# Performance work log

Measured on AMD Instinct MI355X. Metric: run time of the kernel, lower is better.

## Reference

```python
import jax, jax.numpy as jnp
import numpy as np

N_NODES = 100000
N_EDGES = 3200000
BATCH = 256
NUM_TAU = 4
ORDER = 8


def setup_inputs() -> dict:
    key = jax.random.key(0)
    k1, k2, k3, k4, k5 = jax.random.split(key, 5)
    coeffs = jax.random.normal(k1, (NUM_TAU, ORDER + 1), dtype=jnp.float32)
    # positive weights mimicking a degree-normalized adjacency
    edge_weights = jax.random.uniform(k2, (N_EDGES,), dtype=jnp.float32)
    src = jax.random.randint(k3, (N_EDGES,), 0, N_NODES, dtype=jnp.int32)
    dst = jax.random.randint(k4, (N_EDGES,), 0, N_NODES, dtype=jnp.int32)
    batch_indices = jax.random.randint(k5, (BATCH,), 0, N_NODES, dtype=jnp.int64)
    return {
        "coeffs": coeffs,
        "edge_weights": edge_weights,
        "src": src,
        "dst": dst,
        "batch_indices": batch_indices,
        "n_nodes": N_NODES,
    }


def reference(coeffs, edge_weights, src, dst, batch_indices, n_nodes):
    # coeffs: [num_tau, order+1]; edge list defines sparse normalized adjacency.
    B = batch_indices.shape[0]
    order = coeffs.shape[1] - 1
    # _create_batch: one-hot columns, monome[batch_indices[j], j] = 1
    monome = jnp.zeros((n_nodes, B), dtype=coeffs.dtype)
    monome = monome.at[batch_indices, jnp.arange(B)].set(1.0)
    # out[t] = sum_k coeffs[t, k] * A^k @ one_hot
    out = coeffs[:, 0][:, None, None] * monome[None, :, :]
    for k in range(order):
        # SpMM: monome_new[d] += w_e * monome[s] for each edge e=(s,d)
        monome = jax.ops.segment_sum(
            edge_weights[:, None] * monome[src], dst, num_segments=n_nodes
        )
        out = out + coeffs[:, k + 1][:, None, None] * monome[None, :, :]
    return out
```

## Files before the change

### kernel.cpp

```cpp
#include <hip/hip_runtime.h>

#define N_NODES 100000
#define BATCH   256
#define NUM_TAU 4
#define ORDER   8
#define NB      ((size_t)N_NODES * BATCH)
#define NBUK    98
#define NBLK    391

__device__ __forceinline__ unsigned short f2bf(float f) {
    unsigned int u = __float_as_uint(f);
    u += 0x7FFFu + ((u >> 16) & 1u);
    return (unsigned short)(u >> 16);
}
__device__ __forceinline__ float bf2f(unsigned short h) {
    return __uint_as_float((unsigned int)h << 16);
}


__global__ void hist_kernel(const int* __restrict__ dst, int* __restrict__ counts, int E) {
    int e = blockIdx.x * blockDim.x + threadIdx.x;
    if (e < E) atomicAdd(&counts[dst[e]], 1);
}

__global__ void scan1(const int* __restrict__ counts, int* __restrict__ blockSum) {
    __shared__ int s[256];
    int n = blockIdx.x * 256 + threadIdx.x;
    s[threadIdx.x] = (n < N_NODES) ? counts[n] : 0;
    __syncthreads();
    for (int st = 128; st > 0; st >>= 1) {
        if (threadIdx.x < st) s[threadIdx.x] += s[threadIdx.x + st];
        __syncthreads();
    }
    if (threadIdx.x == 0) blockSum[blockIdx.x] = s[0];
}

__global__ void scan2(int* __restrict__ blockSum) {
    __shared__ int s[512];
    int t = threadIdx.x;
    int v = (t < NBLK) ? blockSum[t] : 0;
    s[t] = v;
    __syncthreads();
    for (int st = 1; st < 512; st <<= 1) {
        int u = (t >= st) ? s[t - st] : 0;
        __syncthreads();
        s[t] += u;
        __syncthreads();
    }
    if (t < NBLK) blockSum[t] = s[t] - v;
}

__global__ void scan3(const int* __restrict__ counts, const int* __restrict__ blockSumEx,
                      int* __restrict__ rowStart) {
    __shared__ int s[256];
    int n = blockIdx.x * 256 + threadIdx.x;
    int v = (n < N_NODES) ? counts[n] : 0;
    s[threadIdx.x] = v;
    __syncthreads();
    for (int st = 1; st < 256; st <<= 1) {
        int u = (threadIdx.x >= st) ? s[threadIdx.x - st] : 0;
        __syncthreads();
        s[threadIdx.x] += u;
        __syncthreads();
    }
    if (n < N_NODES) rowStart[n] = blockSumEx[blockIdx.x] + s[threadIdx.x] - v;
}

__global__ void initcur_kernel(const int* __restrict__ rowStart, int* __restrict__ cursor,
                               int* __restrict__ bcur) {
    int n = blockIdx.x * 256 + threadIdx.x;
    if (n < N_NODES) cursor[n] = rowStart[n];
    if (n < NBUK) bcur[n] = rowStart[n << 10];
}

#define EPT 16
__global__ void bucketize_kernel(const int* __restrict__ src, const int* __restrict__ dst,
                                 const float* __restrict__ w, int* __restrict__ bcur,
                                 int2* __restrict__ isw, int* __restrict__ idn, int E) {
    __shared__ int cnt[NBUK], base[NBUK], off[NBUK];
    int e0 = blockIdx.x * (256 * EPT);
    for (int i = threadIdx.x; i < NBUK; i += 256) { cnt[i] = 0; off[i] = 0; }
    __syncthreads();
    #pragma unroll
    for (int i = 0; i < EPT; ++i) {
        int e = e0 + i * 256 + threadIdx.x;
        if (e < E) atomicAdd(&cnt[dst[e] >> 10], 1);
    }
    __syncthreads();
    for (int i = threadIdx.x; i < NBUK; i += 256) {
        int c = cnt[i];
        base[i] = c ? atomicAdd(&bcur[i], c) : 0;
    }
    __syncthreads();
    #pragma unroll
    for (int i = 0; i < EPT; ++i) {
        int e = e0 + i * 256 + threadIdx.x;
        if (e < E) {
            int d = dst[e];
            int b = d >> 10;
            int p = base[b] + atomicAdd(&off[b], 1);
            isw[p] = make_int2(src[e], __float_as_int(w[e]));
            idn[p] = d;
        }
    }
}

__global__ void place_kernel(const int2* __restrict__ isw, const int* __restrict__ idn,
                             int* __restrict__ cursor, int2* __restrict__ csr_pair, int E) {
    int e = blockIdx.x * blockDim.x + threadIdx.x;
    if (e < E) {
        int d = idn[e];
        int p = atomicAdd(&cursor[d], 1);
        csr_pair[p] = isw[e];
    }
}


__global__ void colmap_kernel(const int* __restrict__ bi, int* __restrict__ col_of_node,
                              int* __restrict__ next_dup) {
    int j = threadIdx.x;
    int prev = atomicExch(&col_of_node[bi[j]], j);
    next_dup[j] = prev;
}

__global__ void m1_edges_kernel(const int* __restrict__ src, const int* __restrict__ dst,
                                const float* __restrict__ w,
                                const int* __restrict__ col_of_node,
                                const int* __restrict__ next_dup,
                                float* __restrict__ m1, int* __restrict__ flag, int E) {
    int e = blockIdx.x * blockDim.x + threadIdx.x;
    if (e >= E) return;
    int j = col_of_node[src[e]];
    if (j < 0) return;
    float we = w[e];
    int d = dst[e];
    flag[d] = 1;
    size_t rb = (size_t)d * BATCH;
    while (j >= 0) {
        atomicAdd(&m1[rb + j], we);
        j = next_dup[j];
    }
}

__global__ void spmm_k2(const float* __restrict__ m1, unsigned short* __restrict__ m2,
                        const int* __restrict__ rowStart, const int* __restrict__ counts,
                        const int2* __restrict__ csr_pair, const int* __restrict__ flag) {
    int wave = threadIdx.x >> 6;
    int lane = threadIdx.x & 63;
    int node = blockIdx.x * 4 + wave;
    if (node >= N_NODES) return;
    int col0 = lane * 4;

    int start = rowStart[node];
    int len   = counts[node];

    float4 acc = make_float4(0.f, 0.f, 0.f, 0.f);
    for (int i = 0; i < len; ++i) {
        int2 pr = csr_pair[start + i];
        if (flag[pr.x]) {
            float w = __int_as_float(pr.y);
            float4 v = *(const float4*)(m1 + (size_t)pr.x * BATCH + col0);
            acc.x += w * v.x; acc.y += w * v.y; acc.z += w * v.z; acc.w += w * v.w;
        }
    }
    ushort4 o;
    o.x = f2bf(acc.x); o.y = f2bf(acc.y); o.z = f2bf(acc.z); o.w = f2bf(acc.w);
    *(ushort4*)(m2 + (size_t)node * BATCH + col0) = o;
}

__global__ void spmm_bf(const unsigned short* __restrict__ min_, unsigned short* __restrict__ mout,
                        const int* __restrict__ rowStart, const int* __restrict__ counts,
                        const int2* __restrict__ csr_pair) {
    int wave = threadIdx.x >> 6;
    int lane = threadIdx.x & 63;
    int node = blockIdx.x * 4 + wave;
    if (node >= N_NODES) return;
    int col0 = lane * 4;

    int start = rowStart[node];
    int len   = counts[node];

    float4 acc = make_float4(0.f, 0.f, 0.f, 0.f);
    int i = 0;
    for (; i + 8 <= len; i += 8) {
        int2 pr[8];
        #pragma unroll
        for (int u = 0; u < 8; ++u) pr[u] = csr_pair[start + i + u];
        ushort4 v[8];
        #pragma unroll
        for (int u = 0; u < 8; ++u)
            v[u] = *(const ushort4*)(min_ + (size_t)pr[u].x * BATCH + col0);
        #pragma unroll
        for (int u = 0; u < 8; ++u) {
            float w = __int_as_float(pr[u].y);
            acc.x += w * bf2f(v[u].x);
            acc.y += w * bf2f(v[u].y);
            acc.z += w * bf2f(v[u].z);
            acc.w += w * bf2f(v[u].w);
        }
    }
    for (; i < len; ++i) {
        int2 pr = csr_pair[start + i];
        float w = __int_as_float(pr.y);
        ushort4 v = *(const ushort4*)(min_ + (size_t)pr.x * BATCH + col0);
        acc.x += w * bf2f(v.x);
        acc.y += w * bf2f(v.y);
        acc.z += w * bf2f(v.z);
        acc.w += w * bf2f(v.w);
    }
    ushort4 o;
    o.x = f2bf(acc.x); o.y = f2bf(acc.y); o.z = f2bf(acc.z); o.w = f2bf(acc.w);
    *(ushort4*)(mout + (size_t)node * BATCH + col0) = o;
}

__global__ void combine_bf(float* __restrict__ out, const unsigned short* __restrict__ m28,
                           const float* __restrict__ coeffs, const int* __restrict__ bi) {
    size_t tid = (size_t)blockIdx.x * blockDim.x + threadIdx.x;
    size_t base = tid * 4;
    if (base >= NB) return;
    int node = (int)(base >> 8);
    int j0   = (int)(base & 255);

    float4 p[ORDER];
    p[0] = *(const float4*)(out + base);
    #pragma unroll
    for (int k = 2; k <= ORDER; ++k) {
        ushort4 v = *(const ushort4*)(m28 + (size_t)(k - 2) * NB + base);
        p[k - 1] = make_float4(bf2f(v.x), bf2f(v.y), bf2f(v.z), bf2f(v.w));
    }

    float oh[4];
    #pragma unroll
    for (int i = 0; i < 4; ++i) oh[i] = (bi[j0 + i] == node) ? 1.0f : 0.0f;

    #pragma unroll
    for (int t = 0; t < NUM_TAU; ++t) {
        float c0 = coeffs[t * (ORDER + 1)];
        float4 o = make_float4(c0 * oh[0], c0 * oh[1], c0 * oh[2], c0 * oh[3]);
        #pragma unroll
        for (int k = 1; k <= ORDER; ++k) {
            float c = coeffs[t * (ORDER + 1) + k];
            o.x += c * p[k - 1].x;
            o.y += c * p[k - 1].y;
            o.z += c * p[k - 1].z;
            o.w += c * p[k - 1].w;
        }
        *(float4*)(out + (size_t)t * NB + base) = o;
    }
}


__global__ void spmm_half(const float* __restrict__ min_, float* __restrict__ mout,
                          const int* __restrict__ rowStart, const int* __restrict__ counts,
                          const int2* __restrict__ csr_pair, int colOff) {
    int wave = threadIdx.x >> 6;
    int lane = threadIdx.x & 63;
    int node = blockIdx.x * 4 + wave;
    if (node >= N_NODES) return;
    int c = colOff + lane * 2;
    int start = rowStart[node];
    int len   = counts[node];
    float2 acc = make_float2(0.f, 0.f);
    int i = 0;
    for (; i + 8 <= len; i += 8) {
        int2 pr[8];
        #pragma unroll
        for (int u = 0; u < 8; ++u) pr[u] = csr_pair[start + i + u];
        float2 v[8];
        #pragma unroll
        for (int u = 0; u < 8; ++u)
            v[u] = *(const float2*)(min_ + (size_t)pr[u].x * BATCH + c);
        #pragma unroll
        for (int u = 0; u < 8; ++u) {
            float w = __int_as_float(pr[u].y);
            acc.x += w * v[u].x;
            acc.y += w * v[u].y;
        }
    }
    for (; i < len; ++i) {
        int2 pr = csr_pair[start + i];
        float w = __int_as_float(pr.y);
        float2 v = *(const float2*)(min_ + (size_t)pr.x * BATCH + c);
        acc.x += w * v.x;
        acc.y += w * v.y;
    }
    *(float2*)(mout + (size_t)node * BATCH + c) = acc;
}

__global__ void combine_kernel(float* __restrict__ out, const float* __restrict__ m14,
                               const float* __restrict__ coeffs, const int* __restrict__ bi) {
    size_t tid = (size_t)blockIdx.x * blockDim.x + threadIdx.x;
    size_t base = tid * 4;
    if (base >= NB) return;
    int node = (int)(base >> 8);
    int j0   = (int)(base & 255);
    float4 p[ORDER];
    #pragma unroll
    for (int k = 1; k <= 4; ++k)
        p[k - 1] = *(const float4*)(m14 + (size_t)(k - 1) * NB + base);
    #pragma unroll
    for (int k = 5; k <= 8; ++k)
        p[k - 1] = *(const float4*)(out + (size_t)(k - 5) * NB + base);
    float oh[4];
    #pragma unroll
    for (int i = 0; i < 4; ++i) oh[i] = (bi[j0 + i] == node) ? 1.0f : 0.0f;
    #pragma unroll
    for (int t = 0; t < NUM_TAU; ++t) {
        float c0 = coeffs[t * (ORDER + 1)];
        float4 o = make_float4(c0 * oh[0], c0 * oh[1], c0 * oh[2], c0 * oh[3]);
        #pragma unroll
        for (int k = 1; k <= ORDER; ++k) {
            float c = coeffs[t * (ORDER + 1) + k];
            o.x += c * p[k - 1].x;
            o.y += c * p[k - 1].y;
            o.z += c * p[k - 1].z;
            o.w += c * p[k - 1].w;
        }
        *(float4*)(out + (size_t)t * NB + base) = o;
    }
}

extern "C" void kernel_launch(void* const* d_in, const int* in_sizes, int n_in,
                              void* d_out, int out_size, void* d_ws, size_t ws_size,
                              hipStream_t stream) {
    const float* coeffs = (const float*)d_in[0];
    const float* ew     = (const float*)d_in[1];
    const int*   src    = (const int*)d_in[2];
    const int*   dst    = (const int*)d_in[3];
    const int*   bi     = (const int*)d_in[4];
    const int E = in_sizes[1];

    float* out = (float*)d_out;

    auto align_up = [](uintptr_t v, uintptr_t a) { return (v + a - 1) & ~(a - 1); };

    uintptr_t p0 = (uintptr_t)d_ws;
    int* counts      = (int*)p0;  p0 += (size_t)N_NODES * 4;  p0 = align_up(p0, 256);
    int* rowStart    = (int*)p0;  p0 += (size_t)N_NODES * 4;  p0 = align_up(p0, 256);
    int* cursor      = (int*)p0;  p0 += (size_t)N_NODES * 4;  p0 = align_up(p0, 256);
    int* blockSum    = (int*)p0;  p0 += (size_t)NBLK * 4;     p0 = align_up(p0, 256);
    int* bcur        = (int*)p0;  p0 += (size_t)NBUK * 4;     p0 = align_up(p0, 256);
    int* col_of_node = (int*)p0;  p0 += (size_t)N_NODES * 4;  p0 = align_up(p0, 256);
    int* next_dup    = (int*)p0;  p0 += 1024;                 p0 = align_up(p0, 256);
    int* flag        = (int*)p0;  p0 += (size_t)N_NODES * 4;  p0 = align_up(p0, 256);
    int2* csr_pair   = (int2*)p0; p0 += (size_t)E * 8;        p0 = align_up(p0, 256);
    void* big        = (void*)p0;
    size_t big_bytes = ((uintptr_t)d_ws + ws_size > p0) ? ((uintptr_t)d_ws + ws_size - p0) : 0;

    int eb = (E + 255) / 256;
    int nodeGrid = (N_NODES + 3) / 4;
    int cgrid = (int)((NB / 4 + 255) / 256);

    bool schemeA = (big_bytes >= 7 * NB * 2);
    uintptr_t ibase;
    if (schemeA) ibase = (uintptr_t)big + 5 * NB * 2;
    else         ibase = (uintptr_t)big + 3 * NB * 4;
    ibase = align_up(ibase, 256);
    int2* isw = (int2*)ibase;
    int*  idn = (int*)(ibase + (size_t)E * 8);

    hipMemsetAsync(counts, 0, (size_t)N_NODES * 4, stream);
    hist_kernel<<<eb, 256, 0, stream>>>(dst, counts, E);
    scan1<<<NBLK, 256, 0, stream>>>(counts, blockSum);
    scan2<<<1, 512, 0, stream>>>(blockSum);
    scan3<<<NBLK, 256, 0, stream>>>(counts, blockSum, rowStart);
    initcur_kernel<<<NBLK, 256, 0, stream>>>(rowStart, cursor, bcur);
    bucketize_kernel<<<(E + 256 * EPT - 1) / (256 * EPT), 256, 0, stream>>>(
        src, dst, ew, bcur, isw, idn, E);
    place_kernel<<<eb, 256, 0, stream>>>(isw, idn, cursor, csr_pair, E);

    if (schemeA) {
        unsigned short* m28 = (unsigned short*)big;
        float* m1 = out;

        hipMemsetAsync(col_of_node, 0xFF, (size_t)N_NODES * 4, stream);
        hipMemsetAsync(flag, 0, (size_t)N_NODES * 4, stream);
        hipMemsetAsync(m1, 0, NB * 4, stream);

        colmap_kernel<<<1, 256, 0, stream>>>(bi, col_of_node, next_dup);
        m1_edges_kernel<<<eb, 256, 0, stream>>>(src, dst, ew, col_of_node, next_dup,
                                                m1, flag, E);
        spmm_k2<<<nodeGrid, 256, 0, stream>>>(m1, m28, rowStart, counts, csr_pair, flag);
        for (int k = 3; k <= ORDER; ++k) {
            spmm_bf<<<nodeGrid, 256, 0, stream>>>(m28 + (size_t)(k - 3) * NB,
                                                  m28 + (size_t)(k - 2) * NB,
                                                  rowStart, counts, csr_pair);
        }
        combine_bf<<<cgrid, 256, 0, stream>>>(out, m28, coeffs, bi);
    } else {
        float* fbig = (float*)big;
        float* mpow[ORDER + 1];
        for (int k = 1; k <= 4; ++k) mpow[k] = fbig + (size_t)(k - 1) * NB;
        for (int k = 5; k <= 8; ++k) mpow[k] = out + (size_t)(k - 5) * NB;

        hipMemsetAsync(col_of_node, 0xFF, (size_t)N_NODES * 4, stream);
        hipMemsetAsync(flag, 0, (size_t)N_NODES * 4, stream);
        hipMemsetAsync(mpow[1], 0, NB * 4, stream);
        colmap_kernel<<<1, 256, 0, stream>>>(bi, col_of_node, next_dup);
        m1_edges_kernel<<<eb, 256, 0, stream>>>(src, dst, ew, col_of_node, next_dup,
                                                mpow[1], flag, E);
        for (int h = 0; h < 2; ++h) {
            int colOff = h * 128;
            for (int k = 2; k <= ORDER; ++k) {
                spmm_half<<<nodeGrid, 256, 0, stream>>>(mpow[k - 1], mpow[k],
                                                        rowStart, counts, csr_pair, colOff);
            }
        }
        combine_kernel<<<cgrid, 256, 0, stream>>>(out, fbig, coeffs, bi);
    }
}
```

Before: 2.022 ms.

## Bucket edges by (dst block, src block) segments so CSR rows are src-sorted

Replaces the per-block dst-bucket scatter with a two-level (dst>>10, src>>10) segment histogram, a per-dst-bucket scan, and a global-atomic scatter into those segments. Edges in each CSR row then come out roughly ordered by source block, which should give the SpMM gathers better cache locality. The cost is a second atomic in the histogram, global atomics on about 9.6k counters in place of shared-memory local offsets, and an extra scan kernel.

```diff
diff --git a/kernel.cpp b/kernel.cpp
--- a/kernel.cpp
+++ b/kernel.cpp
@@ -6,6 +6,7 @@
 #define ORDER   8
 #define NB      ((size_t)N_NODES * BATCH)
 #define NBUK    98
+#define NSEG    (NBUK * NBUK)
 #define NBLK    391
 
 __device__ __forceinline__ unsigned short f2bf(float f) {
@@ -18,9 +19,14 @@
 }
 
 
-__global__ void hist_kernel(const int* __restrict__ dst, int* __restrict__ counts, int E) {
+__global__ void hist_kernel(const int* __restrict__ src, const int* __restrict__ dst,
+                            int* __restrict__ counts, int* __restrict__ segCnt, int E) {
     int e = blockIdx.x * blockDim.x + threadIdx.x;
-    if (e < E) atomicAdd(&counts[dst[e]], 1);
+    if (e < E) {
+        int d = dst[e];
+        atomicAdd(&counts[d], 1);
+        atomicAdd(&segCnt[(d >> 10) * NBUK + (src[e] >> 10)], 1);
+    }
 }
 
 __global__ void scan1(const int* __restrict__ counts, int* __restrict__ blockSum) {
@@ -66,42 +72,37 @@
     if (n < N_NODES) rowStart[n] = blockSumEx[blockIdx.x] + s[threadIdx.x] - v;
 }
 
-__global__ void initcur_kernel(const int* __restrict__ rowStart, int* __restrict__ cursor,
-                               int* __restrict__ bcur) {
+__global__ void initcur_kernel(const int* __restrict__ rowStart, int* __restrict__ cursor) {
     int n = blockIdx.x * 256 + threadIdx.x;
     if (n < N_NODES) cursor[n] = rowStart[n];
-    if (n < NBUK) bcur[n] = rowStart[n << 10];
-}
-
-#define EPT 16
-__global__ void bucketize_kernel(const int* __restrict__ src, const int* __restrict__ dst,
-                                 const float* __restrict__ w, int* __restrict__ bcur,
-                                 int2* __restrict__ isw, int* __restrict__ idn, int E) {
-    __shared__ int cnt[NBUK], base[NBUK], off[NBUK];
-    int e0 = blockIdx.x * (256 * EPT);
-    for (int i = threadIdx.x; i < NBUK; i += 256) { cnt[i] = 0; off[i] = 0; }
+}
+
+__global__ void segscan_kernel(const int* __restrict__ segCnt, const int* __restrict__ rowStart,
+                               int* __restrict__ segCur) {
+    __shared__ int s[128];
+    int b = blockIdx.x;
+    int t = threadIdx.x;
+    int v = (t < NBUK) ? segCnt[b * NBUK + t] : 0;
+    s[t] = v;
     __syncthreads();
-    #pragma unroll
-    for (int i = 0; i < EPT; ++i) {
-        int e = e0 + i * 256 + threadIdx.x;
-        if (e < E) atomicAdd(&cnt[dst[e] >> 10], 1);
-    }
-    __syncthreads();
-    for (int i = threadIdx.x; i < NBUK; i += 256) {
-        int c = cnt[i];
-        base[i] = c ? atomicAdd(&bcur[i], c) : 0;
-    }
-    __syncthreads();
-    #pragma unroll
-    for (int i = 0; i < EPT; ++i) {
-        int e = e0 + i * 256 + threadIdx.x;
-        if (e < E) {
-            int d = dst[e];
-            int b = d >> 10;
-            int p = base[b] + atomicAdd(&off[b], 1);
-            isw[p] = make_int2(src[e], __float_as_int(w[e]));
-            idn[p] = d;
-        }
+    for (int st = 1; st < 128; st <<= 1) {
+        int u = (t >= st) ? s[t - st] : 0;
+        __syncthreads();
+        s[t] += u;
+        __syncthreads();
+    }
+    if (t < NBUK) segCur[b * NBUK + t] = rowStart[b << 10] + s[t] - v;
+}
+
+__global__ void scatter2_kernel(const int* __restrict__ src, const int* __restrict__ dst,
+                                const float* __restrict__ w, int* __restrict__ segCur,
+                                int2* __restrict__ isw, int* __restrict__ idn, int E) {
+    int e = blockIdx.x * blockDim.x + threadIdx.x;
+    if (e < E) {
+        int s0 = src[e], d = dst[e];
+        int p = atomicAdd(&segCur[(d >> 10) * NBUK + (s0 >> 10)], 1);
+        isw[p] = make_int2(s0, __float_as_int(w[e]));
+        idn[p] = d;
     }
 }
 
@@ -339,7 +340,8 @@
     int* rowStart    = (int*)p0;  p0 += (size_t)N_NODES * 4;  p0 = align_up(p0, 256);
     int* cursor      = (int*)p0;  p0 += (size_t)N_NODES * 4;  p0 = align_up(p0, 256);
     int* blockSum    = (int*)p0;  p0 += (size_t)NBLK * 4;     p0 = align_up(p0, 256);
-    int* bcur        = (int*)p0;  p0 += (size_t)NBUK * 4;     p0 = align_up(p0, 256);
+    int* segCnt      = (int*)p0;  p0 += (size_t)NSEG * 4;     p0 = align_up(p0, 256);
+    int* segCur      = (int*)p0;  p0 += (size_t)NSEG * 4;     p0 = align_up(p0, 256);
     int* col_of_node = (int*)p0;  p0 += (size_t)N_NODES * 4;  p0 = align_up(p0, 256);
     int* next_dup    = (int*)p0;  p0 += 1024;                 p0 = align_up(p0, 256);
     int* flag        = (int*)p0;  p0 += (size_t)N_NODES * 4;  p0 = align_up(p0, 256);
@@ -360,13 +362,14 @@
     int*  idn = (int*)(ibase + (size_t)E * 8);
 
     hipMemsetAsync(counts, 0, (size_t)N_NODES * 4, stream);
-    hist_kernel<<<eb, 256, 0, stream>>>(dst, counts, E);
+    hipMemsetAsync(segCnt, 0, (size_t)NSEG * 4, stream);
+    hist_kernel<<<eb, 256, 0, stream>>>(src, dst, counts, segCnt, E);
     scan1<<<NBLK, 256, 0, stream>>>(counts, blockSum);
     scan2<<<1, 512, 0, stream>>>(blockSum);
     scan3<<<NBLK, 256, 0, stream>>>(counts, blockSum, rowStart);
-    initcur_kernel<<<NBLK, 256, 0, stream>>>(rowStart, cursor, bcur);
-    bucketize_kernel<<<(E + 256 * EPT - 1) / (256 * EPT), 256, 0, stream>>>(
-        src, dst, ew, bcur, isw, idn, E);
+    initcur_kernel<<<NBLK, 256, 0, stream>>>(rowStart, cursor);
+    segscan_kernel<<<NBUK, 128, 0, stream>>>(segCnt, rowStart, segCur);
+    scatter2_kernel<<<eb, 256, 0, stream>>>(src, dst, ew, segCur, isw, idn, E);
     place_kernel<<<eb, 256, 0, stream>>>(isw, idn, cursor, csr_pair, E);
 
     if (schemeA) {
```

Result: slower. 2.340 ms (+15.7%).

## Slice bf16 monome buffers into 16-column panels for cache-resident SpMM gathers

Applied to the files above, without the earlier changes.

Stores the bf16 power matrices as 16 column slices of 16 columns each, so each slice (about 3.2 MB) can stay resident in cache while the SpMM kernel gathers neighbor rows. The new SpMM launches slice-major blocks in which each wave handles 12 rows, with lanes split into 8 edge groups by 8 column pairs, followed by a shuffle reduction. The aim is to turn random 512-byte row gathers from a 51 MB matrix into cache-hitting 32-byte gathers. The trade-off is that CSR indices and weights are now re-read once per slice, 16 times in total, and combine and spmm_k2 must use the sliced addressing.

```diff
diff --git a/kernel.cpp b/kernel.cpp
--- a/kernel.cpp
+++ b/kernel.cpp
@@ -7,6 +7,11 @@
 #define NB      ((size_t)N_NODES * BATCH)
 #define NBUK    98
 #define NBLK    391
+#define SLICES  16
+#define SCOLS   16
+#define NB_SL   ((size_t)N_NODES * SCOLS)
+#define RPW     12
+#define CHUNKS  2084
 
 __device__ __forceinline__ unsigned short f2bf(float f) {
     unsigned int u = __float_as_uint(f);
@@ -165,52 +170,65 @@
     }
     ushort4 o;
     o.x = f2bf(acc.x); o.y = f2bf(acc.y); o.z = f2bf(acc.z); o.w = f2bf(acc.w);
-    *(ushort4*)(m2 + (size_t)node * BATCH + col0) = o;
-}
-
-__global__ void spmm_bf(const unsigned short* __restrict__ min_, unsigned short* __restrict__ mout,
-                        const int* __restrict__ rowStart, const int* __restrict__ counts,
-                        const int2* __restrict__ csr_pair) {
+    int slice = col0 >> 4;
+    int off   = col0 & 15;
+    *(ushort4*)(m2 + (size_t)slice * NB_SL + (size_t)node * SCOLS + off) = o;
+}
+
+__global__ void spmm_bf_slice(const unsigned short* __restrict__ min_,
+                              unsigned short* __restrict__ mout,
+                              const int* __restrict__ rowStart, const int* __restrict__ counts,
+                              const int2* __restrict__ csr_pair) {
+    int slice = blockIdx.x / CHUNKS;
+    int chunk = blockIdx.x - slice * CHUNKS;
     int wave = threadIdx.x >> 6;
     int lane = threadIdx.x & 63;
-    int node = blockIdx.x * 4 + wave;
-    if (node >= N_NODES) return;
-    int col0 = lane * 4;
-
-    int start = rowStart[node];
-    int len   = counts[node];
-
-    float4 acc = make_float4(0.f, 0.f, 0.f, 0.f);
-    int i = 0;
-    for (; i + 8 <= len; i += 8) {
-        int2 pr[8];
-        #pragma unroll
-        for (int u = 0; u < 8; ++u) pr[u] = csr_pair[start + i + u];
-        ushort4 v[8];
-        #pragma unroll
-        for (int u = 0; u < 8; ++u)
-            v[u] = *(const ushort4*)(min_ + (size_t)pr[u].x * BATCH + col0);
-        #pragma unroll
-        for (int u = 0; u < 8; ++u) {
-            float w = __int_as_float(pr[u].y);
-            acc.x += w * bf2f(v[u].x);
-            acc.y += w * bf2f(v[u].y);
-            acc.z += w * bf2f(v[u].z);
-            acc.w += w * bf2f(v[u].w);
-        }
-    }
-    for (; i < len; ++i) {
-        int2 pr = csr_pair[start + i];
-        float w = __int_as_float(pr.y);
-        ushort4 v = *(const ushort4*)(min_ + (size_t)pr.x * BATCH + col0);
-        acc.x += w * bf2f(v.x);
-        acc.y += w * bf2f(v.y);
-        acc.z += w * bf2f(v.z);
-        acc.w += w * bf2f(v.w);
-    }
-    ushort4 o;
-    o.x = f2bf(acc.x); o.y = f2bf(acc.y); o.z = f2bf(acc.z); o.w = f2bf(acc.w);
-    *(ushort4*)(mout + (size_t)node * BATCH + col0) = o;
+    int g = lane >> 3;
+    int c = lane & 7;
+
+    const unsigned short* msl = min_ + (size_t)slice * NB_SL;
+    unsigned short*       osl = mout + (size_t)slice * NB_SL;
+
+    int node0 = (chunk * 4 + wave) * RPW;
+    for (int r = 0; r < RPW; ++r) {
+        int node = node0 + r;
+        if (node >= N_NODES) return;
+        int start = rowStart[node];
+        int len   = counts[node];
+        float ax = 0.f, ay = 0.f;
+        int i = 0;
+        for (; i + 32 <= len; i += 32) {
+            int2 pr0 = csr_pair[start + i + g];
+            int2 pr1 = csr_pair[start + i + 8 + g];
+            int2 pr2 = csr_pair[start + i + 16 + g];
+            int2 pr3 = csr_pair[start + i + 24 + g];
+            unsigned int v0 = *(const unsigned int*)(msl + (size_t)pr0.x * SCOLS + c * 2);
+            unsigned int v1 = *(const unsigned int*)(msl + (size_t)pr1.x * SCOLS + c * 2);
+            unsigned int v2 = *(const unsigned int*)(msl + (size_t)pr2.x * SCOLS + c * 2);
+            unsigned int v3 = *(const unsigned int*)(msl + (size_t)pr3.x * SCOLS + c * 2);
+            float w0 = __int_as_float(pr0.y), w1 = __int_as_float(pr1.y);
+            float w2 = __int_as_float(pr2.y), w3 = __int_as_float(pr3.y);
+            ax += w0 * bf2f((unsigned short)v0); ay += w0 * bf2f((unsigned short)(v0 >> 16));
+            ax += w1 * bf2f((unsigned short)v1); ay += w1 * bf2f((unsigned short)(v1 >> 16));
+            ax += w2 * bf2f((unsigned short)v2); ay += w2 * bf2f((unsigned short)(v2 >> 16));
+            ax += w3 * bf2f((unsigned short)v3); ay += w3 * bf2f((unsigned short)(v3 >> 16));
+        }
+        for (; i < len; i += 8) {
+            int e = i + g;
+            int s0 = 0; float w = 0.f;
+            if (e < len) { int2 pr = csr_pair[start + e]; s0 = pr.x; w = __int_as_float(pr.y); }
+            unsigned int v = *(const unsigned int*)(msl + (size_t)s0 * SCOLS + c * 2);
+            ax += w * bf2f((unsigned short)v);
+            ay += w * bf2f((unsigned short)(v >> 16));
+        }
+        ax += __shfl_xor(ax, 8);  ay += __shfl_xor(ay, 8);
+        ax += __shfl_xor(ax, 16); ay += __shfl_xor(ay, 16);
+        ax += __shfl_xor(ax, 32); ay += __shfl_xor(ay, 32);
+        if (g == 0) {
+            unsigned int o = ((unsigned int)f2bf(ay) << 16) | (unsigned int)f2bf(ax);
+            *(unsigned int*)(osl + (size_t)node * SCOLS + c * 2) = o;
+        }
+    }
 }
 
 __global__ void combine_bf(float* __restrict__ out, const unsigned short* __restrict__ m28,
@@ -220,12 +238,15 @@
     if (base >= NB) return;
     int node = (int)(base >> 8);
     int j0   = (int)(base & 255);
+    int slice = j0 >> 4;
+    int off   = j0 & 15;
+    size_t sbase = (size_t)slice * NB_SL + (size_t)node * SCOLS + off;
 
     float4 p[ORDER];
     p[0] = *(const float4*)(out + base);
     #pragma unroll
     for (int k = 2; k <= ORDER; ++k) {
-        ushort4 v = *(const ushort4*)(m28 + (size_t)(k - 2) * NB + base);
+        ushort4 v = *(const ushort4*)(m28 + (size_t)(k - 2) * NB + sbase);
         p[k - 1] = make_float4(bf2f(v.x), bf2f(v.y), bf2f(v.z), bf2f(v.w));
     }
 
@@ -382,9 +403,9 @@
                                                 m1, flag, E);
         spmm_k2<<<nodeGrid, 256, 0, stream>>>(m1, m28, rowStart, counts, csr_pair, flag);
         for (int k = 3; k <= ORDER; ++k) {
-            spmm_bf<<<nodeGrid, 256, 0, stream>>>(m28 + (size_t)(k - 3) * NB,
-                                                  m28 + (size_t)(k - 2) * NB,
-                                                  rowStart, counts, csr_pair);
+            spmm_bf_slice<<<SLICES * CHUNKS, 256, 0, stream>>>(
+                m28 + (size_t)(k - 3) * NB, m28 + (size_t)(k - 2) * NB,
+                rowStart, counts, csr_pair);
         }
         combine_bf<<<cgrid, 256, 0, stream>>>(out, m28, coeffs, bi);
     } else {
```

New measurement: 4.125 ms. +104.0%, slower.

## Build CSR per bucket in shared memory and fuse last SpMM with combine

Applied to the files above, without the earlier changes.

CSR construction no longer does a global per-node histogram, a three-kernel scan and global-atomic placement. Edges are now bucketed by 1024-node ranges, and each bucket's per-node counts, prefix sums and placement are done in one block using shared-memory atomics. The last SpMM step is fused with the coefficient combine, so the eighth power is never written in bf16 and read back, and one scratch buffer goes away. The fused kernel reads m1 only when the node's flag is set, which relies on m1 being zero elsewhere. Building the CSR takes only 98 blocks, which may leave most of the GPU idle during that stage.

```diff
diff --git a/kernel.cpp b/kernel.cpp
--- a/kernel.cpp
+++ b/kernel.cpp
@@ -6,7 +6,7 @@
 #define ORDER   8
 #define NB      ((size_t)N_NODES * BATCH)
 #define NBUK    98
-#define NBLK    391
+#define EPT     16
 
 __device__ __forceinline__ unsigned short f2bf(float f) {
     unsigned int u = __float_as_uint(f);
@@ -18,62 +18,38 @@
 }
 
 
-__global__ void hist_kernel(const int* __restrict__ dst, int* __restrict__ counts, int E) {
-    int e = blockIdx.x * blockDim.x + threadIdx.x;
-    if (e < E) atomicAdd(&counts[dst[e]], 1);
-}
-
-__global__ void scan1(const int* __restrict__ counts, int* __restrict__ blockSum) {
-    __shared__ int s[256];
-    int n = blockIdx.x * 256 + threadIdx.x;
-    s[threadIdx.x] = (n < N_NODES) ? counts[n] : 0;
-    __syncthreads();
-    for (int st = 128; st > 0; st >>= 1) {
-        if (threadIdx.x < st) s[threadIdx.x] += s[threadIdx.x + st];
-        __syncthreads();
-    }
-    if (threadIdx.x == 0) blockSum[blockIdx.x] = s[0];
-}
-
-__global__ void scan2(int* __restrict__ blockSum) {
-    __shared__ int s[512];
+__global__ void bukhist_kernel(const int* __restrict__ dst, int* __restrict__ bukCnt, int E) {
+    __shared__ int c[NBUK];
+    for (int i = threadIdx.x; i < NBUK; i += 256) c[i] = 0;
+    __syncthreads();
+    int e0 = blockIdx.x * (256 * EPT);
+    #pragma unroll
+    for (int i = 0; i < EPT; ++i) {
+        int e = e0 + i * 256 + threadIdx.x;
+        if (e < E) atomicAdd(&c[dst[e] >> 10], 1);
+    }
+    __syncthreads();
+    for (int i = threadIdx.x; i < NBUK; i += 256)
+        if (c[i]) atomicAdd(&bukCnt[i], c[i]);
+}
+
+__global__ void bukscan_kernel(const int* __restrict__ bukCnt, int* __restrict__ bukBase,
+                               int* __restrict__ bcur, int E) {
+    __shared__ int s[128];
     int t = threadIdx.x;
-    int v = (t < NBLK) ? blockSum[t] : 0;
+    int v = (t < NBUK) ? bukCnt[t] : 0;
     s[t] = v;
     __syncthreads();
-    for (int st = 1; st < 512; st <<= 1) {
+    for (int st = 1; st < 128; st <<= 1) {
         int u = (t >= st) ? s[t - st] : 0;
         __syncthreads();
         s[t] += u;
         __syncthreads();
     }
-    if (t < NBLK) blockSum[t] = s[t] - v;
-}
-
-__global__ void scan3(const int* __restrict__ counts, const int* __restrict__ blockSumEx,
-                      int* __restrict__ rowStart) {
-    __shared__ int s[256];
-    int n = blockIdx.x * 256 + threadIdx.x;
-    int v = (n < N_NODES) ? counts[n] : 0;
-    s[threadIdx.x] = v;
-    __syncthreads();
-    for (int st = 1; st < 256; st <<= 1) {
-        int u = (threadIdx.x >= st) ? s[threadIdx.x - st] : 0;
-        __syncthreads();
-        s[threadIdx.x] += u;
-        __syncthreads();
-    }
-    if (n < N_NODES) rowStart[n] = blockSumEx[blockIdx.x] + s[threadIdx.x] - v;
-}
-
-__global__ void initcur_kernel(const int* __restrict__ rowStart, int* __restrict__ cursor,
-                               int* __restrict__ bcur) {
-    int n = blockIdx.x * 256 + threadIdx.x;
-    if (n < N_NODES) cursor[n] = rowStart[n];
-    if (n < NBUK) bcur[n] = rowStart[n << 10];
-}
-
-#define EPT 16
+    if (t < NBUK) { int ex = s[t] - v; bukBase[t] = ex; bcur[t] = ex; }
+    if (t == 0) bukBase[NBUK] = E;
+}
+
 __global__ void bucketize_kernel(const int* __restrict__ src, const int* __restrict__ dst,
                                  const float* __restrict__ w, int* __restrict__ bcur,
                                  int2* __restrict__ isw, int* __restrict__ idn, int E) {
@@ -105,12 +81,50 @@
     }
 }
 
-__global__ void place_kernel(const int2* __restrict__ isw, const int* __restrict__ idn,
-                             int* __restrict__ cursor, int2* __restrict__ csr_pair, int E) {
-    int e = blockIdx.x * blockDim.x + threadIdx.x;
-    if (e < E) {
+__global__ void buildcsr_kernel(const int2* __restrict__ isw, const int* __restrict__ idn,
+                                const int* __restrict__ bukBase,
+                                int* __restrict__ counts, int* __restrict__ rowStart,
+                                int2* __restrict__ csr_pair) {
+    __shared__ int cnt[1024];
+    __shared__ int part[256];
+    int b = blockIdx.x;
+    int n0 = b << 10;
+    int nN = N_NODES - n0; if (nN > 1024) nN = 1024;
+    int e0 = bukBase[b], e1 = bukBase[b + 1];
+    int t = threadIdx.x;
+
+    #pragma unroll
+    for (int i = t; i < 1024; i += 256) cnt[i] = 0;
+    __syncthreads();
+    for (int e = e0 + t; e < e1; e += 256)
+        atomicAdd(&cnt[idn[e] - n0], 1);
+    __syncthreads();
+
+    int i0 = t * 4;
+    int c0 = cnt[i0], c1 = cnt[i0 + 1], c2 = cnt[i0 + 2], c3 = cnt[i0 + 3];
+    int sum = c0 + c1 + c2 + c3;
+    part[t] = sum;
+    __syncthreads();
+    int v = sum;
+    for (int st = 1; st < 256; st <<= 1) {
+        int u = (t >= st) ? part[t - st] : 0;
+        __syncthreads();
+        part[t] += u;
+        __syncthreads();
+    }
+    int ex = part[t] - v;
+
+    int o0 = ex, o1 = ex + c0, o2 = o1 + c1, o3 = o2 + c2;
+    if (i0 + 0 < nN) { counts[n0 + i0 + 0] = c0; rowStart[n0 + i0 + 0] = e0 + o0; }
+    if (i0 + 1 < nN) { counts[n0 + i0 + 1] = c1; rowStart[n0 + i0 + 1] = e0 + o1; }
+    if (i0 + 2 < nN) { counts[n0 + i0 + 2] = c2; rowStart[n0 + i0 + 2] = e0 + o2; }
+    if (i0 + 3 < nN) { counts[n0 + i0 + 3] = c3; rowStart[n0 + i0 + 3] = e0 + o3; }
+    cnt[i0] = o0; cnt[i0 + 1] = o1; cnt[i0 + 2] = o2; cnt[i0 + 3] = o3;
+    __syncthreads();
+
+    for (int e = e0 + t; e < e1; e += 256) {
         int d = idn[e];
-        int p = atomicAdd(&cursor[d], 1);
+        int p = e0 + atomicAdd(&cnt[d - n0], 1);
         csr_pair[p] = isw[e];
     }
 }
@@ -213,25 +227,64 @@
     *(ushort4*)(mout + (size_t)node * BATCH + col0) = o;
 }
 
-__global__ void combine_bf(float* __restrict__ out, const unsigned short* __restrict__ m28,
-                           const float* __restrict__ coeffs, const int* __restrict__ bi) {
-    size_t tid = (size_t)blockIdx.x * blockDim.x + threadIdx.x;
-    size_t base = tid * 4;
-    if (base >= NB) return;
-    int node = (int)(base >> 8);
-    int j0   = (int)(base & 255);
-
+__global__ void spmm_bf_last(const unsigned short* __restrict__ m27,
+                             const int* __restrict__ rowStart, const int* __restrict__ counts,
+                             const int2* __restrict__ csr_pair,
+                             const float* __restrict__ coeffs, const int* __restrict__ flag,
+                             float* __restrict__ out, const int* __restrict__ bi) {
+    int wave = threadIdx.x >> 6;
+    int lane = threadIdx.x & 63;
+    int node = blockIdx.x * 4 + wave;
+    if (node >= N_NODES) return;
+    int col0 = lane * 4;
+
+    int start = rowStart[node];
+    int len   = counts[node];
+    const unsigned short* m7 = m27 + 5 * NB;
+
+    float4 acc = make_float4(0.f, 0.f, 0.f, 0.f);
+    int i = 0;
+    for (; i + 8 <= len; i += 8) {
+        int2 pr[8];
+        #pragma unroll
+        for (int u = 0; u < 8; ++u) pr[u] = csr_pair[start + i + u];
+        ushort4 v[8];
+        #pragma unroll
+        for (int u = 0; u < 8; ++u)
+            v[u] = *(const ushort4*)(m7 + (size_t)pr[u].x * BATCH + col0);
+        #pragma unroll
+        for (int u = 0; u < 8; ++u) {
+            float w = __int_as_float(pr[u].y);
+            acc.x += w * bf2f(v[u].x);
+            acc.y += w * bf2f(v[u].y);
+            acc.z += w * bf2f(v[u].z);
+            acc.w += w * bf2f(v[u].w);
+        }
+    }
+    for (; i < len; ++i) {
+        int2 pr = csr_pair[start + i];
+        float w = __int_as_float(pr.y);
+        ushort4 v = *(const ushort4*)(m7 + (size_t)pr.x * BATCH + col0);
+        acc.x += w * bf2f(v.x);
+        acc.y += w * bf2f(v.y);
+        acc.z += w * bf2f(v.z);
+        acc.w += w * bf2f(v.w);
+    }
+
+    size_t base = (size_t)node * BATCH + col0;
     float4 p[ORDER];
-    p[0] = *(const float4*)(out + base);
-    #pragma unroll
-    for (int k = 2; k <= ORDER; ++k) {
-        ushort4 v = *(const ushort4*)(m28 + (size_t)(k - 2) * NB + base);
+    if (flag[node]) p[0] = *(const float4*)(out + base);
+    else            p[0] = make_float4(0.f, 0.f, 0.f, 0.f);
+    #pragma unroll
+    for (int k = 2; k <= 7; ++k) {
+        ushort4 v = *(const ushort4*)(m27 + (size_t)(k - 2) * NB + base);
         p[k - 1] = make_float4(bf2f(v.x), bf2f(v.y), bf2f(v.z), bf2f(v.w));
     }
+    p[7] = acc;
 
     float oh[4];
     #pragma unroll
-    for (int i = 0; i < 4; ++i) oh[i] = (bi[j0 + i] == node) ? 1.0f : 0.0f;
+    for (int q = 0; q < 4; ++q) oh[q] = (bi[col0 + q] == node) ? 1.0f : 0.0f;
 
     #pragma unroll
     for (int t = 0; t < NUM_TAU; ++t) {
@@ -337,8 +390,8 @@
     uintptr_t p0 = (uintptr_t)d_ws;
     int* counts      = (int*)p0;  p0 += (size_t)N_NODES * 4;  p0 = align_up(p0, 256);
     int* rowStart    = (int*)p0;  p0 += (size_t)N_NODES * 4;  p0 = align_up(p0, 256);
-    int* cursor      = (int*)p0;  p0 += (size_t)N_NODES * 4;  p0 = align_up(p0, 256);
-    int* blockSum    = (int*)p0;  p0 += (size_t)NBLK * 4;     p0 = align_up(p0, 256);
+    int* bukCnt      = (int*)p0;  p0 += (size_t)NBUK * 4;     p0 = align_up(p0, 256);
+    int* bukBase     = (int*)p0;  p0 += (size_t)(NBUK + 1) * 4; p0 = align_up(p0, 256);
     int* bcur        = (int*)p0;  p0 += (size_t)NBUK * 4;     p0 = align_up(p0, 256);
     int* col_of_node = (int*)p0;  p0 += (size_t)N_NODES * 4;  p0 = align_up(p0, 256);
     int* next_dup    = (int*)p0;  p0 += 1024;                 p0 = align_up(p0, 256);
@@ -348,29 +401,26 @@
     size_t big_bytes = ((uintptr_t)d_ws + ws_size > p0) ? ((uintptr_t)d_ws + ws_size - p0) : 0;
 
     int eb = (E + 255) / 256;
+    int ebt = (E + 256 * EPT - 1) / (256 * EPT);
     int nodeGrid = (N_NODES + 3) / 4;
     int cgrid = (int)((NB / 4 + 255) / 256);
 
-    bool schemeA = (big_bytes >= 7 * NB * 2);
+    bool schemeA = (big_bytes >= 6 * NB * 2);
     uintptr_t ibase;
-    if (schemeA) ibase = (uintptr_t)big + 5 * NB * 2;
+    if (schemeA) ibase = (uintptr_t)big + 4 * NB * 2;
     else         ibase = (uintptr_t)big + 3 * NB * 4;
     ibase = align_up(ibase, 256);
     int2* isw = (int2*)ibase;
     int*  idn = (int*)(ibase + (size_t)E * 8);
 
-    hipMemsetAsync(counts, 0, (size_t)N_NODES * 4, stream);
-    hist_kernel<<<eb, 256, 0, stream>>>(dst, counts, E);
-    scan1<<<NBLK, 256, 0, stream>>>(counts, blockSum);
-    scan2<<<1, 512, 0, stream>>>(blockSum);
-    scan3<<<NBLK, 256, 0, stream>>>(counts, blockSum, rowStart);
-    initcur_kernel<<<NBLK, 256, 0, stream>>>(rowStart, cursor, bcur);
-    bucketize_kernel<<<(E + 256 * EPT - 1) / (256 * EPT), 256, 0, stream>>>(
-        src, dst, ew, bcur, isw, idn, E);
-    place_kernel<<<eb, 256, 0, stream>>>(isw, idn, cursor, csr_pair, E);
+    hipMemsetAsync(bukCnt, 0, (size_t)NBUK * 4, stream);
+    bukhist_kernel<<<ebt, 256, 0, stream>>>(dst, bukCnt, E);
+    bukscan_kernel<<<1, 128, 0, stream>>>(bukCnt, bukBase, bcur, E);
+    bucketize_kernel<<<ebt, 256, 0, stream>>>(src, dst, ew, bcur, isw, idn, E);
+    buildcsr_kernel<<<NBUK, 256, 0, stream>>>(isw, idn, bukBase, counts, rowStart, csr_pair);
 
     if (schemeA) {
-        unsigned short* m28 = (unsigned short*)big;
+        unsigned short* m27 = (unsigned short*)big;
         float* m1 = out;
 
         hipMemsetAsync(col_of_node, 0xFF, (size_t)N_NODES * 4, stream);
@@ -380,13 +430,14 @@
         colmap_kernel<<<1, 256, 0, stream>>>(bi, col_of_node, next_dup);
         m1_edges_kernel<<<eb, 256, 0, stream>>>(src, dst, ew, col_of_node, next_dup,
                                                 m1, flag, E);
-        spmm_k2<<<nodeGrid, 256, 0, stream>>>(m1, m28, rowStart, counts, csr_pair, flag);
-        for (int k = 3; k <= ORDER; ++k) {
-            spmm_bf<<<nodeGrid, 256, 0, stream>>>(m28 + (size_t)(k - 3) * NB,
-                                                  m28 + (size_t)(k - 2) * NB,
+        spmm_k2<<<nodeGrid, 256, 0, stream>>>(m1, m27, rowStart, counts, csr_pair, flag);
+        for (int k = 3; k <= 7; ++k) {
+            spmm_bf<<<nodeGrid, 256, 0, stream>>>(m27 + (size_t)(k - 3) * NB,
+                                                  m27 + (size_t)(k - 2) * NB,
                                                   rowStart, counts, csr_pair);
         }
-        combine_bf<<<cgrid, 256, 0, stream>>>(out, m28, coeffs, bi);
+        spmm_bf_last<<<nodeGrid, 256, 0, stream>>>(m27, rowStart, counts, csr_pair,
+                                                   coeffs, flag, out, bi);
     } else {
         float* fbig = (float*)big;
         float* mpow[ORDER + 1];
```

Measured after the change: 1.864 ms. -7.8%, faster.
